# Kernel optimization log

Measured on AMD Instinct MI355X. Metric: run time of the kernel, lower is better.

Reference implementation:

```python
import math
import jax, jax.numpy as jnp
import numpy as np

B, N, D = 16384, 16, 2
HIDDEN, DL = 64, 5
OMEGA = 1.0
CUSP_GAMMA = 1.0 / (D - 1)  # dim=2 -> 1.0


def _linear_params(key, fan_in, fan_out):
    kw, kb = jax.random.split(key)
    bound = 1.0 / math.sqrt(fan_in)
    w = jax.random.uniform(kw, (fan_out, fan_in), jnp.float32, -bound, bound)
    b = jax.random.uniform(kb, (fan_out,), jnp.float32, -bound, bound)
    return w, b


def setup_inputs() -> dict:
    key = jax.random.key(0)
    ks = jax.random.split(key, 9)
    x = jax.random.normal(ks[0], (B, N, D), jnp.float32)
    phi_w0, phi_b0 = _linear_params(ks[1], D + 1, HIDDEN)
    phi_w1, phi_b1 = _linear_params(ks[2], HIDDEN, HIDDEN)
    phi_w2, phi_b2 = _linear_params(ks[3], HIDDEN, DL)
    psi_w0, psi_b0 = _linear_params(ks[4], 6, HIDDEN)
    psi_w1, psi_b1 = _linear_params(ks[5], HIDDEN, HIDDEN)
    psi_w2, psi_b2 = _linear_params(ks[6], HIDDEN, DL)
    rho_w0, rho_b0 = _linear_params(ks[7], 2 * DL, HIDDEN)
    # rho output layer: weight std=0.01 normal, bias zeros (matches torch init)
    rho_w1 = 0.01 * jax.random.normal(ks[8], (1, HIDDEN), jnp.float32)
    rho_b1 = jnp.zeros((1,), jnp.float32)
    return dict(x=x,
                phi_w0=phi_w0, phi_b0=phi_b0, phi_w1=phi_w1, phi_b1=phi_b1,
                phi_w2=phi_w2, phi_b2=phi_b2,
                psi_w0=psi_w0, psi_b0=psi_b0, psi_w1=psi_w1, psi_b1=psi_b1,
                psi_w2=psi_w2, psi_b2=psi_b2,
                rho_w0=rho_w0, rho_b0=rho_b0, rho_w1=rho_w1, rho_b1=rho_b1)


def _mlp3(h, w0, b0, w1, b1, w2, b2):
    h = jax.nn.gelu(h @ w0.T + b0, approximate=False)
    h = jax.nn.gelu(h @ w1.T + b1, approximate=False)
    return h @ w2.T + b2


def reference(x, phi_w0, phi_b0, phi_w1, phi_b1, phi_w2, phi_b2,
              psi_w0, psi_b0, psi_w1, psi_b1, psi_w2, psi_b2,
              rho_w0, rho_b0, rho_w1, rho_b1):
    # one-body branch
    xs = x * math.sqrt(OMEGA)                       # [B,N,D]
    r2 = (xs ** 2).sum(-1, keepdims=True)           # [B,N,1]
    phi_in = jnp.concatenate([xs, r2], -1)          # [B,N,D+1]
    phi_out = _mlp3(phi_in, phi_w0, phi_b0, phi_w1, phi_b1, phi_w2, phi_b2).mean(1)  # [B,dL]

    # two-body branch: vectorized over all N*(N-1)/2 pairs
    ii, jj = jnp.triu_indices(N, k=1)               # static pair index lists, P entries
    dr = x[:, ii, :] - x[:, jj, :]                  # [B,P,D]
    rij = jnp.sqrt((dr ** 2).sum(-1) + 1e-12)       # [B,P]
    feat = jnp.stack([jnp.log1p(rij), rij / (1 + rij), jnp.exp(-rij ** 2),
                      jnp.exp(-0.5 * rij), jnp.exp(-rij), jnp.exp(-2 * rij)], -1)  # [B,P,6]
    psi_out = _mlp3(feat, psi_w0, psi_b0, psi_w1, psi_b1, psi_w2, psi_b2).mean(1)  # [B,dL]
    cusp = CUSP_GAMMA * (rij * jnp.exp(-rij)).sum(-1)  # [B]

    # readout
    rho_in = jnp.concatenate([phi_out, psi_out], -1)   # [B,2*dL]
    h = jax.nn.gelu(rho_in @ rho_w0.T + rho_b0, approximate=False)
    f = (h @ rho_w1.T + rho_b1).squeeze(-1)            # [B]
    return f + cusp
```

## Files before the change

kernel.cpp:

```cpp
#include <hip/hip_runtime.h>
#include <hip/hip_bf16.h>
#include <math.h>

#define B_TOT 16384
#define NPART 16
#define NPAIR 120
#define HID   64
#define DL    5
#define GB    2
#define PSI_BL 120
#define PHI_ROW 240
#define NROW  272

typedef __attribute__((ext_vector_type(8))) short short8;
typedef __attribute__((ext_vector_type(4))) float floatx4;

__device__ __forceinline__ float gelu_sig(float v) {
    float e = __expf(-1.702f * v);
    return v * __builtin_amdgcn_rcpf(1.0f + e);
}

__device__ __forceinline__ unsigned pk2(float a, float b) {
    __hip_bfloat162 h = __float22bfloat162_rn(make_float2(a, b));
    union { __hip_bfloat162 h; unsigned u; } cv; cv.h = h;
    return cv.u;
}

__device__ __forceinline__ unsigned short f2bfbits(float f) {
    __hip_bfloat16 h = __float2bfloat16(f);
    union { __hip_bfloat16 h; unsigned short u; } cv; cv.h = h;
    return cv.u;
}

__device__ __forceinline__ float wred(float v) {
    v += __shfl_down(v, 32);
    v += __shfl_down(v, 16);
    v += __shfl_down(v, 8);
    v += __shfl_down(v, 4);
    v += __shfl_down(v, 2);
    v += __shfl_down(v, 1);
    return v;
}

__global__ __launch_bounds__(256) void jastrow_mfma5(
    const float* __restrict__ x,
    const float* __restrict__ phi_w0, const float* __restrict__ phi_b0,
    const float* __restrict__ phi_w1, const float* __restrict__ phi_b1,
    const float* __restrict__ phi_w2, const float* __restrict__ phi_b2,
    const float* __restrict__ psi_w0, const float* __restrict__ psi_b0,
    const float* __restrict__ psi_w1, const float* __restrict__ psi_b1,
    const float* __restrict__ psi_w2, const float* __restrict__ psi_b2,
    const float* __restrict__ rho_w0, const float* __restrict__ rho_b0,
    const float* __restrict__ rho_w1, const float* __restrict__ rho_b1,
    float* __restrict__ out)
{
    const int t    = threadIdx.x;
    const int lane = t & 63;
    const int wv   = t >> 6;
    const int q    = lane >> 4;
    const int m15  = lane & 15;
    const int bg   = blockIdx.x * GB;

    __shared__ __align__(16) unsigned short s_h[NROW * 64];
    __shared__ __align__(16) unsigned char  s_mem[4352];
    __shared__ float s_cusp[4];

    unsigned short* s_f  = (unsigned short*)s_mem;
    float*          s_cs = (float*)s_mem;

    const float2* x2 = (const float2*)x;
    float cusp = 0.f;

    {
        const int bl = t >> 7;
        const int p  = t & 127;
        if (p < NPAIR) {
            int u = 119 - p;
            float sq = sqrtf((float)(8 * u + 1));
            int k = (int)((sq - 1.0f) * 0.5f);
            int i = 14 - k;
            int j = p - (i * (31 - i)) / 2 + i + 1;

            float2 xi = x2[(bg + bl) * NPART + i];
            float2 xj = x2[(bg + bl) * NPART + j];
            float dx = xi.x - xj.x, dy = xi.y - xj.y;
            float r = sqrtf(dx * dx + dy * dy + 1e-12f);

            float f0 = __logf(1.f + r);
            float f1 = r * __builtin_amdgcn_rcpf(1.f + r);
            float f2 = __expf(-r * r);
            float f3 = __expf(-0.5f * r);
            float f4 = __expf(-r);
            float f5 = f4 * f4;
            cusp = r * f4;

            union { short8 s; unsigned u4[4]; } v;
            v.u4[0] = pk2(f0, f1);
            v.u4[1] = pk2(f2, f3);
            v.u4[2] = pk2(f4, f5);
            v.u4[3] = 0u;
            *(short8*)&s_f[(bl * PSI_BL + p) * 8] = v.s;
        }
        if (t < GB * NPART) {
            int bl2 = t >> 4, n = t & 15;
            float2 xv = x2[(bg + bl2) * NPART + n];
            float r2 = xv.x * xv.x + xv.y * xv.y;
            union { short8 s; unsigned u4[4]; } w;
            w.u4[0] = pk2(xv.x, xv.y);
            w.u4[1] = pk2(r2, 0.f);
            w.u4[2] = 0u; w.u4[3] = 0u;
            *(short8*)&s_f[(PHI_ROW + t) * 8] = w.s;
        }
    }
    __syncthreads();

    const int colb = wv * 16 + m15;
    int swz[4];
#pragma unroll
    for (int rg = 0; rg < 4; ++rg) swz[rg] = colb ^ (((q * 4 + rg) & 7) << 3);

    {
        short8 Bp1 = (short8)0, Bf1 = (short8)0;
        if (q == 0) {
            union { short8 s; unsigned u4[4]; } bb;
            const float* w = psi_w0 + colb * 6;
            bb.u4[0] = pk2(w[0], w[1]); bb.u4[1] = pk2(w[2], w[3]);
            bb.u4[2] = pk2(w[4], w[5]); bb.u4[3] = 0u;
            Bp1 = bb.s;
            const float* wf = phi_w0 + colb * 3;
            bb.u4[0] = pk2(wf[0], wf[1]); bb.u4[1] = pk2(wf[2], 0.f);
            bb.u4[2] = 0u; bb.u4[3] = 0u;
            Bf1 = bb.s;
        }
        float b0p = psi_b0[colb];
        float b0f = phi_b0[colb];
        floatx4 Cp = {b0p, b0p, b0p, b0p};
        floatx4 Cf = {b0f, b0f, b0f, b0f};

#pragma unroll
        for (int bl = 0; bl < GB; ++bl)
#pragma unroll
            for (int Mt = 0; Mt < 8; ++Mt) {
                int rowbase = bl * PSI_BL + Mt * 16;
                short8 a = (short8)0;
                if (q == 0) a = *(const short8*)&s_f[(rowbase + m15) * 8];
                floatx4 d = __builtin_amdgcn_mfma_f32_16x16x32_bf16(a, Bp1, Cp, 0, 0, 0);
                if (Mt < 7 || q < 2) {
#pragma unroll
                    for (int rg = 0; rg < 4; ++rg)
                        s_h[(rowbase + q * 4 + rg) * 64 + swz[rg]] =
                            f2bfbits(gelu_sig(d[rg]));
                }
            }
#pragma unroll
        for (int bl = 0; bl < GB; ++bl) {
            int rowbase = PHI_ROW + bl * 16;
            short8 a = (short8)0;
            if (q == 0) a = *(const short8*)&s_f[(rowbase + m15) * 8];
            floatx4 d = __builtin_amdgcn_mfma_f32_16x16x32_bf16(a, Bf1, Cf, 0, 0, 0);
#pragma unroll
            for (int rg = 0; rg < 4; ++rg)
                s_h[(rowbase + q * 4 + rg) * 64 + swz[rg]] =
                    f2bfbits(gelu_sig(d[rg]));
        }
    }
    __syncthreads();

    float csP[GB] = {0.f, 0.f};
    float csF[GB] = {0.f, 0.f};
    {
        short8 Bp2[2], Bf2[2];
#pragma unroll
        for (int Kc = 0; Kc < 2; ++Kc) {
            int k0 = Kc * 32 + q * 8;
            const float* wp = psi_w1 + colb * HID + k0;
            const float* wf = phi_w1 + colb * HID + k0;
            union { short8 s; unsigned u4[4]; } bp, bf;
#pragma unroll
            for (int e2 = 0; e2 < 4; ++e2) {
                bp.u4[e2] = pk2(wp[e2 * 2], wp[e2 * 2 + 1]);
                bf.u4[e2] = pk2(wf[e2 * 2], wf[e2 * 2 + 1]);
            }
            Bp2[Kc] = bp.s; Bf2[Kc] = bf.s;
        }
        float b1p = psi_b1[colb];
        float b1f = phi_b1[colb];
        floatx4 Cp = {b1p, b1p, b1p, b1p};
        floatx4 Cf = {b1f, b1f, b1f, b1f};

        const int h  = m15 & 7;
        const int g0 = (q ^ h) << 3;
        const int g1 = g0 ^ 32;

#pragma unroll
        for (int bl = 0; bl < GB; ++bl)
#pragma unroll
            for (int Mt = 0; Mt < 8; ++Mt) {
                int rb = (bl * PSI_BL + Mt * 16 + m15) * 64;
                short8 a0 = *(const short8*)&s_h[rb + g0];
                short8 a1 = *(const short8*)&s_h[rb + g1];
                floatx4 acc = __builtin_amdgcn_mfma_f32_16x16x32_bf16(a0, Bp2[0], Cp, 0, 0, 0);
                acc = __builtin_amdgcn_mfma_f32_16x16x32_bf16(a1, Bp2[1], acc, 0, 0, 0);
                if (Mt == 7) {
                    if (q < 2) {
#pragma unroll
                        for (int rg = 0; rg < 4; ++rg)
                            csP[bl] += gelu_sig(acc[rg]);
                    }
                } else {
#pragma unroll
                    for (int rg = 0; rg < 4; ++rg)
                        csP[bl] += gelu_sig(acc[rg]);
                }
            }
#pragma unroll
        for (int bl = 0; bl < GB; ++bl) {
            int rb = (PHI_ROW + bl * 16 + m15) * 64;
            short8 a0 = *(const short8*)&s_h[rb + g0];
            short8 a1 = *(const short8*)&s_h[rb + g1];
            floatx4 acc = __builtin_amdgcn_mfma_f32_16x16x32_bf16(a0, Bf2[0], Cf, 0, 0, 0);
            acc = __builtin_amdgcn_mfma_f32_16x16x32_bf16(a1, Bf2[1], acc, 0, 0, 0);
#pragma unroll
            for (int rg = 0; rg < 4; ++rg)
                csF[bl] += gelu_sig(acc[rg]);
        }
    }
#pragma unroll
    for (int bl = 0; bl < GB; ++bl) {
        s_cs[(((0 * GB + bl) * 4 + wv) * 4 + q) * 16 + m15] = csP[bl];
        s_cs[(((1 * GB + bl) * 4 + wv) * 4 + q) * 16 + m15] = csF[bl];
    }
    {
        float cc = wred(cusp);
        if (lane == 0) s_cusp[wv] = cc;
    }
    __syncthreads();

    if (t < 128) {
        const int blr = wv;
        const int c   = lane;
        const int cw  = c >> 4, cm = c & 15;
        float colP = 0.f, colF = 0.f;
#pragma unroll
        for (int qq = 0; qq < 4; ++qq) {
            colP += s_cs[(((0 * GB + blr) * 4 + cw) * 4 + qq) * 16 + cm];
            colF += s_cs[(((1 * GB + blr) * 4 + cw) * 4 + qq) * 16 + cm];
        }

        float psiv[DL], phiv[DL];
#pragma unroll
        for (int d = 0; d < DL; ++d) {
            float sP = wred(colP * psi_w2[d * HID + c]);
            psiv[d] = __shfl(sP, 0) * (1.0f / NPAIR) + psi_b2[d];
            float sF = wred(colF * phi_w2[d * HID + c]);
            phiv[d] = __shfl(sF, 0) * (1.0f / NPART) + phi_b2[d];
        }

        int j = lane;
        float a = rho_b0[j];
        const float* wr = rho_w0 + j * (2 * DL);
#pragma unroll
        for (int d = 0; d < DL; ++d)
            a += phiv[d] * wr[d] + psiv[d] * wr[DL + d];
        float cuspb = s_cusp[2 * blr] + s_cusp[2 * blr + 1];
        float cv = gelu_sig(a) * rho_w1[j];
        cv = wred(cv);
        if (j == 0) out[bg + blr] = cv + rho_b1[0] + cuspb;
    }
}

extern "C" void kernel_launch(void* const* d_in, const int* in_sizes, int n_in,
                              void* d_out, int out_size, void* d_ws, size_t ws_size,
                              hipStream_t stream) {
    const float* x      = (const float*)d_in[0];
    const float* phi_w0 = (const float*)d_in[1];
    const float* phi_b0 = (const float*)d_in[2];
    const float* phi_w1 = (const float*)d_in[3];
    const float* phi_b1 = (const float*)d_in[4];
    const float* phi_w2 = (const float*)d_in[5];
    const float* phi_b2 = (const float*)d_in[6];
    const float* psi_w0 = (const float*)d_in[7];
    const float* psi_b0 = (const float*)d_in[8];
    const float* psi_w1 = (const float*)d_in[9];
    const float* psi_b1 = (const float*)d_in[10];
    const float* psi_w2 = (const float*)d_in[11];
    const float* psi_b2 = (const float*)d_in[12];
    const float* rho_w0 = (const float*)d_in[13];
    const float* rho_b0 = (const float*)d_in[14];
    const float* rho_w1 = (const float*)d_in[15];
    const float* rho_b1 = (const float*)d_in[16];

    jastrow_mfma5<<<B_TOT / GB, 256, 0, stream>>>(
        x,
        phi_w0, phi_b0, phi_w1, phi_b1, phi_w2, phi_b2,
        psi_w0, psi_b0, psi_w1, psi_b1, psi_w2, psi_b2,
        rho_w0, rho_b0, rho_w1, rho_b1,
        (float*)d_out);
}
```

Measured before the change: 188.5 us.

## Process batch elements sequentially to halve hidden-activation LDS buffer

The hidden-layer LDS buffer shrinks from 272 to 136 rows by running layer 1 and layer 2 once per batch element instead of across both at once. The layer-2 weight loads are hoisted ahead of the first barrier so they overlap with feature computation. The aim is lower LDS use per block, which lets more blocks fit per CU. In exchange, each block now runs more barriers (two per batch element) and has less independent MFMA work in flight between them.

```diff
diff --git a/kernel.cpp b/kernel.cpp
--- a/kernel.cpp
+++ b/kernel.cpp
@@ -8,9 +8,10 @@
 #define HID   64
 #define DL    5
 #define GB    2
-#define PSI_BL 120
-#define PHI_ROW 240
-#define NROW  272
+#define PSI_ROWS 120
+#define PHI_HROW 120
+#define NROW_IT  136
+#define SF_PHI   240
 
 typedef __attribute__((ext_vector_type(8))) short short8;
 typedef __attribute__((ext_vector_type(4))) float floatx4;
@@ -42,7 +43,7 @@
     return v;
 }
 
-__global__ __launch_bounds__(256) void jastrow_mfma5(
+__global__ __launch_bounds__(256) void jastrow_mfma6(
     const float* __restrict__ x,
     const float* __restrict__ phi_w0, const float* __restrict__ phi_b0,
     const float* __restrict__ phi_w1, const float* __restrict__ phi_b1,
@@ -61,7 +62,7 @@
     const int m15  = lane & 15;
     const int bg   = blockIdx.x * GB;
 
-    __shared__ __align__(16) unsigned short s_h[NROW * 64];
+    __shared__ __align__(16) unsigned short s_h[NROW_IT * 64];
     __shared__ __align__(16) unsigned char  s_mem[4352];
     __shared__ float s_cusp[4];
 
@@ -99,7 +100,7 @@
             v.u4[1] = pk2(f2, f3);
             v.u4[2] = pk2(f4, f5);
             v.u4[3] = 0u;
-            *(short8*)&s_f[(bl * PSI_BL + p) * 8] = v.s;
+            *(short8*)&s_f[(bl * PSI_ROWS + p) * 8] = v.s;
         }
         if (t < GB * NPART) {
             int bl2 = t >> 4, n = t & 15;
@@ -109,122 +110,114 @@
             w.u4[0] = pk2(xv.x, xv.y);
             w.u4[1] = pk2(r2, 0.f);
             w.u4[2] = 0u; w.u4[3] = 0u;
-            *(short8*)&s_f[(PHI_ROW + t) * 8] = w.s;
-        }
-    }
-    __syncthreads();
+            *(short8*)&s_f[(SF_PHI + t) * 8] = w.s;
+        }
+    }
 
     const int colb = wv * 16 + m15;
     int swz[4];
 #pragma unroll
     for (int rg = 0; rg < 4; ++rg) swz[rg] = colb ^ (((q * 4 + rg) & 7) << 3);
 
-    {
-        short8 Bp1 = (short8)0, Bf1 = (short8)0;
-        if (q == 0) {
-            union { short8 s; unsigned u4[4]; } bb;
-            const float* w = psi_w0 + colb * 6;
-            bb.u4[0] = pk2(w[0], w[1]); bb.u4[1] = pk2(w[2], w[3]);
-            bb.u4[2] = pk2(w[4], w[5]); bb.u4[3] = 0u;
-            Bp1 = bb.s;
-            const float* wf = phi_w0 + colb * 3;
-            bb.u4[0] = pk2(wf[0], wf[1]); bb.u4[1] = pk2(wf[2], 0.f);
-            bb.u4[2] = 0u; bb.u4[3] = 0u;
-            Bf1 = bb.s;
-        }
-        float b0p = psi_b0[colb];
-        float b0f = phi_b0[colb];
-        floatx4 Cp = {b0p, b0p, b0p, b0p};
-        floatx4 Cf = {b0f, b0f, b0f, b0f};
-
-#pragma unroll
-        for (int bl = 0; bl < GB; ++bl)
-#pragma unroll
-            for (int Mt = 0; Mt < 8; ++Mt) {
-                int rowbase = bl * PSI_BL + Mt * 16;
-                short8 a = (short8)0;
-                if (q == 0) a = *(const short8*)&s_f[(rowbase + m15) * 8];
-                floatx4 d = __builtin_amdgcn_mfma_f32_16x16x32_bf16(a, Bp1, Cp, 0, 0, 0);
-                if (Mt < 7 || q < 2) {
-#pragma unroll
-                    for (int rg = 0; rg < 4; ++rg)
-                        s_h[(rowbase + q * 4 + rg) * 64 + swz[rg]] =
-                            f2bfbits(gelu_sig(d[rg]));
-                }
-            }
-#pragma unroll
-        for (int bl = 0; bl < GB; ++bl) {
-            int rowbase = PHI_ROW + bl * 16;
-            short8 a = (short8)0;
-            if (q == 0) a = *(const short8*)&s_f[(rowbase + m15) * 8];
-            floatx4 d = __builtin_amdgcn_mfma_f32_16x16x32_bf16(a, Bf1, Cf, 0, 0, 0);
-#pragma unroll
-            for (int rg = 0; rg < 4; ++rg)
-                s_h[(rowbase + q * 4 + rg) * 64 + swz[rg]] =
-                    f2bfbits(gelu_sig(d[rg]));
-        }
-    }
-    __syncthreads();
+    short8 Bp1 = (short8)0, Bf1 = (short8)0;
+    if (q == 0) {
+        union { short8 s; unsigned u4[4]; } bb;
+        const float* w = psi_w0 + colb * 6;
+        bb.u4[0] = pk2(w[0], w[1]); bb.u4[1] = pk2(w[2], w[3]);
+        bb.u4[2] = pk2(w[4], w[5]); bb.u4[3] = 0u;
+        Bp1 = bb.s;
+        const float* wf = phi_w0 + colb * 3;
+        bb.u4[0] = pk2(wf[0], wf[1]); bb.u4[1] = pk2(wf[2], 0.f);
+        bb.u4[2] = 0u; bb.u4[3] = 0u;
+        Bf1 = bb.s;
+    }
+    float b0p = psi_b0[colb], b0f = phi_b0[colb];
+    floatx4 C0p = {b0p, b0p, b0p, b0p};
+    floatx4 C0f = {b0f, b0f, b0f, b0f};
+
+    short8 Bp2[2], Bf2[2];
+#pragma unroll
+    for (int Kc = 0; Kc < 2; ++Kc) {
+        int k0 = Kc * 32 + q * 8;
+        const float* wp = psi_w1 + colb * HID + k0;
+        const float* wf = phi_w1 + colb * HID + k0;
+        union { short8 s; unsigned u4[4]; } bp, bf;
+#pragma unroll
+        for (int e2 = 0; e2 < 4; ++e2) {
+            bp.u4[e2] = pk2(wp[e2 * 2], wp[e2 * 2 + 1]);
+            bf.u4[e2] = pk2(wf[e2 * 2], wf[e2 * 2 + 1]);
+        }
+        Bp2[Kc] = bp.s; Bf2[Kc] = bf.s;
+    }
+    float b1p = psi_b1[colb], b1f = phi_b1[colb];
+    floatx4 C1p = {b1p, b1p, b1p, b1p};
+    floatx4 C1f = {b1f, b1f, b1f, b1f};
+
+    const int g0 = ((q ^ (m15 & 7)) << 3);
+    const int g1 = g0 ^ 32;
 
     float csP[GB] = {0.f, 0.f};
     float csF[GB] = {0.f, 0.f};
-    {
-        short8 Bp2[2], Bf2[2];
-#pragma unroll
-        for (int Kc = 0; Kc < 2; ++Kc) {
-            int k0 = Kc * 32 + q * 8;
-            const float* wp = psi_w1 + colb * HID + k0;
-            const float* wf = phi_w1 + colb * HID + k0;
-            union { short8 s; unsigned u4[4]; } bp, bf;
-#pragma unroll
-            for (int e2 = 0; e2 < 4; ++e2) {
-                bp.u4[e2] = pk2(wp[e2 * 2], wp[e2 * 2 + 1]);
-                bf.u4[e2] = pk2(wf[e2 * 2], wf[e2 * 2 + 1]);
+
+    __syncthreads();
+
+#pragma unroll
+    for (int bl = 0; bl < GB; ++bl) {
+#pragma unroll
+        for (int Mt = 0; Mt < 8; ++Mt) {
+            short8 a = (short8)0;
+            if (q == 0) a = *(const short8*)&s_f[(bl * PSI_ROWS + Mt * 16 + m15) * 8];
+            floatx4 d = __builtin_amdgcn_mfma_f32_16x16x32_bf16(a, Bp1, C0p, 0, 0, 0);
+            if (Mt < 7 || q < 2) {
+#pragma unroll
+                for (int rg = 0; rg < 4; ++rg)
+                    s_h[(Mt * 16 + q * 4 + rg) * 64 + swz[rg]] =
+                        f2bfbits(gelu_sig(d[rg]));
             }
-            Bp2[Kc] = bp.s; Bf2[Kc] = bf.s;
-        }
-        float b1p = psi_b1[colb];
-        float b1f = phi_b1[colb];
-        floatx4 Cp = {b1p, b1p, b1p, b1p};
-        floatx4 Cf = {b1f, b1f, b1f, b1f};
-
-        const int h  = m15 & 7;
-        const int g0 = (q ^ h) << 3;
-        const int g1 = g0 ^ 32;
-
-#pragma unroll
-        for (int bl = 0; bl < GB; ++bl)
-#pragma unroll
-            for (int Mt = 0; Mt < 8; ++Mt) {
-                int rb = (bl * PSI_BL + Mt * 16 + m15) * 64;
-                short8 a0 = *(const short8*)&s_h[rb + g0];
-                short8 a1 = *(const short8*)&s_h[rb + g1];
-                floatx4 acc = __builtin_amdgcn_mfma_f32_16x16x32_bf16(a0, Bp2[0], Cp, 0, 0, 0);
-                acc = __builtin_amdgcn_mfma_f32_16x16x32_bf16(a1, Bp2[1], acc, 0, 0, 0);
-                if (Mt == 7) {
-                    if (q < 2) {
-#pragma unroll
-                        for (int rg = 0; rg < 4; ++rg)
-                            csP[bl] += gelu_sig(acc[rg]);
-                    }
-                } else {
+        }
+        {
+            short8 a = (short8)0;
+            if (q == 0) a = *(const short8*)&s_f[(SF_PHI + bl * 16 + m15) * 8];
+            floatx4 d = __builtin_amdgcn_mfma_f32_16x16x32_bf16(a, Bf1, C0f, 0, 0, 0);
+#pragma unroll
+            for (int rg = 0; rg < 4; ++rg)
+                s_h[(PHI_HROW + q * 4 + rg) * 64 + swz[rg]] =
+                    f2bfbits(gelu_sig(d[rg]));
+        }
+        __syncthreads();
+
+#pragma unroll
+        for (int Mt = 0; Mt < 8; ++Mt) {
+            int rb = (Mt * 16 + m15) * 64;
+            short8 a0 = *(const short8*)&s_h[rb + g0];
+            short8 a1 = *(const short8*)&s_h[rb + g1];
+            floatx4 acc = __builtin_amdgcn_mfma_f32_16x16x32_bf16(a0, Bp2[0], C1p, 0, 0, 0);
+            acc = __builtin_amdgcn_mfma_f32_16x16x32_bf16(a1, Bp2[1], acc, 0, 0, 0);
+            if (Mt == 7) {
+                if (q < 2) {
 #pragma unroll
                     for (int rg = 0; rg < 4; ++rg)
                         csP[bl] += gelu_sig(acc[rg]);
                 }
+            } else {
+#pragma unroll
+                for (int rg = 0; rg < 4; ++rg)
+                    csP[bl] += gelu_sig(acc[rg]);
             }
-#pragma unroll
-        for (int bl = 0; bl < GB; ++bl) {
-            int rb = (PHI_ROW + bl * 16 + m15) * 64;
+        }
+        {
+            int rb = (PHI_HROW + m15) * 64;
             short8 a0 = *(const short8*)&s_h[rb + g0];
             short8 a1 = *(const short8*)&s_h[rb + g1];
-            floatx4 acc = __builtin_amdgcn_mfma_f32_16x16x32_bf16(a0, Bf2[0], Cf, 0, 0, 0);
+            floatx4 acc = __builtin_amdgcn_mfma_f32_16x16x32_bf16(a0, Bf2[0], C1f, 0, 0, 0);
             acc = __builtin_amdgcn_mfma_f32_16x16x32_bf16(a1, Bf2[1], acc, 0, 0, 0);
 #pragma unroll
             for (int rg = 0; rg < 4; ++rg)
                 csF[bl] += gelu_sig(acc[rg]);
         }
-    }
+        __syncthreads();
+    }
+
 #pragma unroll
     for (int bl = 0; bl < GB; ++bl) {
         s_cs[(((0 * GB + bl) * 4 + wv) * 4 + q) * 16 + m15] = csP[bl];
@@ -290,7 +283,7 @@
     const float* rho_w1 = (const float*)d_in[15];
     const float* rho_b1 = (const float*)d_in[16];
 
-    jastrow_mfma5<<<B_TOT / GB, 256, 0, stream>>>(
+    jastrow_mfma6<<<B_TOT / GB, 256, 0, stream>>>(
         x,
         phi_w0, phi_b0, phi_w1, phi_b1, phi_w2, phi_b2,
         psi_w0, psi_b0, psi_w1, psi_b1, psi_w2, psi_b2,
```

Result: faster. 182.5 us (-3.2%).
